# Kernel optimization log

Hardware: AMD Instinct MI355X
Metric: run time of the kernel (lower is better)

Reference implementation:

```python
import jax, jax.numpy as jnp
import numpy as np

B, IN, HID, H = 8192, 1024, 2048, 8
UP = 2 * IN          # input_size * proj_factor
HS = HID // H        # head size = 256
EPS = 1e-5


def _blockdiag(x, w, b):
    # x: [B, UP] -> chunk into H blocks of UP//H, per-block linear to HID//H
    xb = x.reshape(B, H, UP // H)
    y = jnp.einsum('bhi,hio->bho', xb, w)
    return y.reshape(B, HID) + b


def setup_inputs() -> dict:
    key = jax.random.key(0)
    ks = jax.random.split(key, 20)
    rn = lambda k, s: jax.random.normal(k, s, jnp.float32)
    p = lambda k, *s: rn(k, s) * 0.02
    return dict(
        x=rn(ks[0], (B, IN)),
        h_prev=rn(ks[1], (B, HID)), c_prev=rn(ks[2], (B, HID)),
        n_prev=rn(ks[3], (B, HID)), m_prev=rn(ks[4], (B, HID)),
        ln_g=jnp.ones(IN), ln_b=jnp.zeros(IN),
        w_ul=p(ks[5], IN, UP), b_ul=jnp.zeros(UP),
        w_ur=p(ks[6], IN, HID), b_ur=jnp.zeros(HID),
        conv_w=p(ks[7], 4), conv_b=jnp.zeros(()),
        w_skip=p(ks[8], UP, HID), b_skip=jnp.zeros(HID),
        w_q=p(ks[9], H, UP // H, HID // H), b_q=jnp.zeros(HID),
        w_k=p(ks[10], H, UP // H, HID // H), b_k=jnp.zeros(HID),
        w_v=p(ks[11], H, UP // H, HID // H), b_v=jnp.zeros(HID),
        w_i=p(ks[12], UP, HID), b_i=jnp.zeros(HID),
        w_f=p(ks[13], UP, HID), b_f=jnp.zeros(HID),
        w_o=p(ks[14], UP, HID), b_o=jnp.zeros(HID),
        gn_g=jnp.ones(HID), gn_b=jnp.zeros(HID),
        w_down=p(ks[15], HID, IN), b_down=jnp.zeros(IN),
    )


def reference(x, h_prev, c_prev, n_prev, m_prev, ln_g, ln_b,
              w_ul, b_ul, w_ur, b_ur, conv_w, conv_b, w_skip, b_skip,
              w_q, b_q, w_k, b_k, w_v, b_v, w_i, b_i, w_f, b_f, w_o, b_o,
              gn_g, gn_b, w_down, b_down):
    # LayerNorm over features
    mu = x.mean(-1, keepdims=True)
    var = x.var(-1, keepdims=True)
    xn = (x - mu) * jax.lax.rsqrt(var + EPS) * ln_g + ln_b

    xul = xn @ w_ul + b_ul          # [B, UP]
    xur = xn @ w_ur + b_ur          # [B, HID]

    # causal conv1d (kernel 4, 1 channel) along the feature axis, left-pad 3
    xp = jnp.pad(xul, ((0, 0), (3, 0)))
    xc = conv_b + sum(conv_w[j] * xp[:, j:j + UP] for j in range(4))
    xc = jax.nn.silu(xc)            # [B, UP]

    x_skip = xc @ w_skip + b_skip

    q = _blockdiag(xc, w_q, b_q)
    k = _blockdiag(xc, w_k, b_k) / np.sqrt(HS).astype(np.float32)
    v = _blockdiag(xul, w_v, b_v)

    i_t = xc @ w_i + b_i
    f_t = xc @ w_f + b_f
    o = jax.nn.sigmoid(xul @ w_o + b_o)

    m_t = jnp.maximum(f_t + m_prev, i_t)
    i = jnp.exp(i_t - m_t)
    f = jnp.exp(f_t + m_prev - m_t)
    c_t = f * c_prev + i * (v * k)
    n_t = f * n_prev + i * k

    denom = jnp.max(jnp.abs(n_t.T @ q), axis=1)     # [HID]
    h_t = o * (c_t * q) / denom

    # GroupNorm on (N, C), groups = H
    hg = h_t.reshape(B, H, HID // H)
    gm = hg.mean(-1, keepdims=True)
    gv = hg.var(-1, keepdims=True)
    hn = ((hg - gm) * jax.lax.rsqrt(gv + EPS)).reshape(B, HID) * gn_g + gn_b

    out = (hn + x_skip) * jax.nn.silu(xur)
    return out @ w_down + b_down + x, h_t, c_t, n_t, m_t
```

## Files before the change

### kernel.cpp

```cpp
#include <hip/hip_runtime.h>
#include <stdint.h>

#define B_    8192
#define IN_   1024
#define HID_  2048
#define UP_   2048
#define H_    8
#define HS_   256
#define EPS_  1e-5f

typedef __bf16 bf16x8 __attribute__((ext_vector_type(8)));
typedef float f32x4 __attribute__((ext_vector_type(4)));
typedef unsigned short u16x4 __attribute__((ext_vector_type(4)));
typedef unsigned short u16x8 __attribute__((ext_vector_type(8)));

__device__ __forceinline__ unsigned short f2bf(float f) {
  union { float f; unsigned int u; } v; v.f = f;
  unsigned int u = v.u;
  unsigned int r = (u + 0x7fffu + ((u >> 16) & 1u)) >> 16;
  return (unsigned short)r;
}
__device__ __forceinline__ float bf2f(unsigned short h) {
  union { unsigned int u; float f; } v; v.u = ((unsigned int)h) << 16;
  return v.f;
}

__device__ __forceinline__ void gload_lds16(const void* g, void* l) {
  auto gp = reinterpret_cast<const uint32_t __attribute__((address_space(1)))*>(
      reinterpret_cast<uintptr_t>(g));
  auto lp = reinterpret_cast<uint32_t __attribute__((address_space(3)))*>(
      reinterpret_cast<uintptr_t>(l));
  __builtin_amdgcn_global_load_lds(gp, lp, 16, 0, 0);
}

#define SB0 __builtin_amdgcn_sched_barrier(0)

#define PREFETCH_AF(DST, BASE, MI0)                                         \
  DST[0][0] = *(const bf16x8*)((BASE) + (aRdBase + (MI0) * 2048));          \
  DST[0][1] = *(const bf16x8*)((BASE) + ((aRdBase + (MI0) * 2048) ^ 64));   \
  DST[1][0] = *(const bf16x8*)((BASE) + (aRdBase + ((MI0) + 1) * 2048));    \
  DST[1][1] = *(const bf16x8*)((BASE) + ((aRdBase + ((MI0) + 1) * 2048) ^ 64));

#define LOAD_BFR(BASE)                                                      \
  _Pragma("unroll")                                                         \
  for (int ni = 0; ni < 4; ++ni) {                                          \
    bfr[ni][0] = *(const bf16x8*)((BASE) + (bRdBase + ni * 2048));          \
    bfr[ni][1] = *(const bf16x8*)((BASE) + ((bRdBase + ni * 2048) ^ 64));   \
  }

#define MFMA_CLUSTER(AF, Q)                                                 \
  __builtin_amdgcn_s_setprio(1);                                           \
  _Pragma("unroll")                                                         \
  for (int kq = 0; kq < 2; ++kq)                                            \
    _Pragma("unroll")                                                       \
    for (int m2 = 0; m2 < 2; ++m2)                                          \
      _Pragma("unroll")                                                     \
      for (int ni = 0; ni < 4; ++ni)                                        \
        acc[(Q) * 2 + m2][ni] = __builtin_amdgcn_mfma_f32_16x16x32_bf16(    \
            AF[m2][kq], bfr[ni][kq], acc[(Q) * 2 + m2][ni], 0, 0, 0);       \
  __builtin_amdgcn_s_setprio(0);

template <typename OutT, bool HAS_ADD>
__global__ __launch_bounds__(512, 2) void gemm8p(
    const unsigned short* __restrict__ A, int lda, int a_zoff,
    const unsigned short* __restrict__ W, int ldw, int w_zoff,
    const float* __restrict__ bias, const float* __restrict__ bias2,
    int bias_zoff,
    OutT* __restrict__ C, OutT* __restrict__ C2, int ldc, int c_zoff,
    int c_split,
    const float* __restrict__ ADD, float scale, float scale2, int K)
{
  __shared__ char lds[163840];
  const int z = blockIdx.z;
  A += (size_t)z * a_zoff;
  W += (size_t)z * w_zoff;
  if (bias) bias += (size_t)z * bias_zoff;
  if (bias2) bias2 += (size_t)z * bias_zoff;

  const int nwg = gridDim.x * gridDim.y;
  const int orig = blockIdx.y * gridDim.x + blockIdx.x;
  const int q8 = nwg >> 3, r8 = nwg & 7;
  const int xcd = orig & 7, xi = orig >> 3;
  const int wg = (xcd < r8 ? xcd * (q8 + 1) : r8 * (q8 + 1) + (xcd - r8) * q8) + xi;
  const int bx = wg % gridDim.x, by = wg / gridDim.x;

  const int t = threadIdx.x;
  const int lane = t & 63, wave = t >> 6;
  const int wr = wave >> 2, wc = wave & 3;
  const int l15 = lane & 15, l4 = lane >> 4;
  const int row0 = by * 256, col0 = bx * 256;

  const int lrow = lane >> 3;
  const int lslot = (lane & 7) ^ lrow;
  const size_t aLane = (size_t)lrow * lda * 2 + (size_t)lslot * 16;
  const size_t wLane = (size_t)lrow * ldw * 2 + (size_t)lslot * 16;
  const char* Abase = (const char*)A;
  const char* Wbase = (const char*)W;

  const int aRdBase = (wr * 128 + l15) * 128 + (((l4) ^ (l15 & 7)) * 16);
  const int bRdBase = (wc * 64 + l15) * 128 + (((l4) ^ (l15 & 7)) * 16);

  auto issueA = [&](int abuf, int half, int tile) {
#pragma unroll
    for (int j = 0; j < 2; ++j) {
      const int rbase = half * 128 + j * 64 + wave * 8;
      gload_lds16(Abase + (size_t)(row0 + rbase) * (lda * 2) + (size_t)tile * 128 + aLane,
                  lds + abuf * 32768 + rbase * 128 + lane * 16);
    }
  };
  auto issueB = [&](int bbuf, int half, int tile) {
#pragma unroll
    for (int j = 0; j < 2; ++j) {
      const int rbase = half * 128 + j * 64 + wave * 8;
      gload_lds16(Wbase + (size_t)(col0 + rbase) * (ldw * 2) + (size_t)tile * 128 + wLane,
                  lds + 98304 + bbuf * 32768 + rbase * 128 + lane * 16);
    }
  };

  f32x4 acc[8][4] = {};
  const int NT = K >> 6;

  bf16x8 bfr[4][2];
  bf16x8 afA[2][2], afB[2][2];

  issueA(0, 0, 0); issueA(0, 1, 0);
  issueB(0, 0, 0); issueB(0, 1, 0);
  if (NT > 1) {
    issueA(1, 0, 1); issueA(1, 1, 1);
    issueB(1, 0, 1); issueB(1, 1, 1);
    asm volatile("s_waitcnt vmcnt(8)" ::: "memory");
  } else {
    asm volatile("s_waitcnt vmcnt(0)" ::: "memory");
  }
  SB0;
  {
    const char* a0 = lds;
    const char* b0 = lds + 98304;
    LOAD_BFR(b0)
    PREFETCH_AF(afA, a0, 0)
    PREFETCH_AF(afB, a0, 2)
  }
  __builtin_amdgcn_s_barrier();
  SB0;

  for (int T = 0; T < NT; ++T) {
    const char* ldsA = lds + (T % 3) * 32768;
    const int abufN = (T + 2) % 3;
    const int bbufN = T & 1;
    asm volatile("s_waitcnt lgkmcnt(4)" ::: "memory"); SB0;
    MFMA_CLUSTER(afA, 0)
    PREFETCH_AF(afA, ldsA, 4)
    if (T + 2 < NT) issueA(abufN, 0, T + 2);
    asm volatile("s_waitcnt lgkmcnt(4)" ::: "memory"); SB0;
    MFMA_CLUSTER(afB, 1)
    __builtin_amdgcn_s_barrier();
    SB0;
    PREFETCH_AF(afB, ldsA, 6)
    if (T + 2 < NT) {
      issueA(abufN, 1, T + 2);
      issueB(bbufN, 0, T + 2);
      issueB(bbufN, 1, T + 2);
    }
    asm volatile("s_waitcnt lgkmcnt(4)" ::: "memory"); SB0;
    MFMA_CLUSTER(afA, 2)
    asm volatile("s_waitcnt lgkmcnt(0)" ::: "memory"); SB0;
    MFMA_CLUSTER(afB, 3)
    if (T + 2 < NT) asm volatile("s_waitcnt vmcnt(8)" ::: "memory");
    else            asm volatile("s_waitcnt vmcnt(0)" ::: "memory");
    SB0;
    if (T + 1 < NT) {
      const char* aN = lds + ((T + 1) % 3) * 32768;
      const char* bN = lds + 98304 + ((T + 1) & 1) * 32768;
      LOAD_BFR(bN)
      PREFETCH_AF(afA, aN, 0)
      PREFETCH_AF(afB, aN, 2)
    }
    __builtin_amdgcn_s_barrier();
    SB0;
  }

  const float* bp = bias;
  OutT* Cp = C;
  int cbase = col0;
  float sc = scale;
  if (col0 >= c_split) { bp = bias2; Cp = C2; cbase = col0 - c_split; sc = scale2; }
#pragma unroll
  for (int mi = 0; mi < 8; ++mi) {
#pragma unroll
    for (int ni = 0; ni < 4; ++ni) {
#pragma unroll
      for (int r = 0; r < 4; ++r) {
        const int m = row0 + wr * 128 + mi * 16 + l4 * 4 + r;
        const int n = wc * 64 + ni * 16 + l15;
        float v = acc[mi][ni][r];
        if (bp) v += bp[cbase + n];
        v *= sc;
        const size_t ci = (size_t)m * ldc + (size_t)z * c_zoff + cbase + n;
        if constexpr (HAS_ADD) v += ADD[ci];
        if constexpr (sizeof(OutT) == 2) Cp[ci] = (OutT)f2bf(v);
        else Cp[ci] = v;
      }
    }
  }
}

__global__ __launch_bounds__(256) void denom_reduce(
    const float* __restrict__ part, float* __restrict__ denom)
{
  const int m = blockIdx.x, t = threadIdx.x;
  const size_t P = (size_t)HID_ * HID_;
  float v = 0.f;
  for (int n = t; n < HID_; n += 256) {
    const size_t o = (size_t)m * HID_ + n;
    float s = part[o] + part[P + o] + part[2 * P + o] + part[3 * P + o];
    v = fmaxf(v, fabsf(s));
  }
#pragma unroll
  for (int off = 1; off < 64; off <<= 1) v = fmaxf(v, __shfl_xor(v, off, 64));
  __shared__ float red[4];
  if ((t & 63) == 0) red[t >> 6] = v;
  __syncthreads();
  if (t == 0) denom[m] = fmaxf(fmaxf(red[0], red[1]), fmaxf(red[2], red[3]));
}

__global__ __launch_bounds__(256) void down_reduce(
    const float* __restrict__ part, const float* __restrict__ x,
    const float* __restrict__ bias, float* __restrict__ out)
{
  const size_t idx = ((size_t)blockIdx.x * 256 + threadIdx.x) * 4;
  const size_t P = (size_t)B_ * IN_;
  f32x4 a = *(const f32x4*)(part + idx);
  f32x4 b = *(const f32x4*)(part + P + idx);
  f32x4 xv = *(const f32x4*)(x + idx);
  const int j = (int)(idx & (IN_ - 1));
  f32x4 bv = *(const f32x4*)(bias + j);
  f32x4 o;
#pragma unroll
  for (int e = 0; e < 4; ++e) o[e] = a[e] + b[e] + bv[e] + xv[e];
  *(f32x4*)(out + idx) = o;
}

template <typename InT>
__global__ __launch_bounds__(256) void transpose_bf(
    const InT* __restrict__ in, unsigned short* __restrict__ out, int R, int C,
    int izoff, int ozoff)
{
  __shared__ float tile[32][33];
  in += (size_t)blockIdx.z * izoff;
  out += (size_t)blockIdx.z * ozoff;
  const int cb = blockIdx.x * 32, rb = blockIdx.y * 32;
  const int tx = threadIdx.x, ty = threadIdx.y;
  for (int i = ty; i < 32; i += 8) {
    InT v = in[(size_t)(rb + i) * C + cb + tx];
    float f;
    if constexpr (sizeof(InT) == 2) f = bf2f((unsigned short)v);
    else f = (float)v;
    tile[i][tx] = f;
  }
  __syncthreads();
  for (int i = ty; i < 32; i += 8)
    out[(size_t)(cb + i) * R + rb + tx] = f2bf(tile[tx][i]);
}

__global__ __launch_bounds__(256) void ln_kernel(
    const float* __restrict__ x, const float* __restrict__ g,
    const float* __restrict__ b, unsigned short* __restrict__ xn)
{
  const int brow = blockIdx.x, t = threadIdx.x;
  const int lane = t & 63, wave = t >> 6;
  const float* xr = x + (size_t)brow * IN_;
  f32x4 v = *(const f32x4*)(xr + t * 4);
  float s = v[0] + v[1] + v[2] + v[3];
  float q = v[0]*v[0] + v[1]*v[1] + v[2]*v[2] + v[3]*v[3];
#pragma unroll
  for (int off = 32; off; off >>= 1) {
    s += __shfl_xor(s, off, 64);
    q += __shfl_xor(q, off, 64);
  }
  __shared__ float ss[4], sq[4];
  if (lane == 0) { ss[wave] = s; sq[wave] = q; }
  __syncthreads();
  s = ss[0] + ss[1] + ss[2] + ss[3];
  q = sq[0] + sq[1] + sq[2] + sq[3];
  const float mean = s * (1.f / IN_);
  const float var = q * (1.f / IN_) - mean * mean;
  const float rs = rsqrtf(var + EPS_);
  u16x4 o;
#pragma unroll
  for (int e = 0; e < 4; ++e) {
    const int j = t * 4 + e;
    o[e] = f2bf((v[e] - mean) * rs * g[j] + b[j]);
  }
  *(u16x4*)(xn + (size_t)brow * IN_ + t * 4) = o;
}

__global__ __launch_bounds__(256) void conv_kernel(
    const unsigned short* __restrict__ xul, const float* __restrict__ cw,
    const float* __restrict__ cb, unsigned short* __restrict__ xc)
{
  const int brow = blockIdx.x, t = threadIdx.x;
  const size_t base = (size_t)brow * UP_;
  const int j0 = t * 8;
  float xv[11];
#pragma unroll
  for (int e = 0; e < 11; ++e) {
    const int j = j0 + e - 3;
    xv[e] = (j >= 0) ? bf2f(xul[base + j]) : 0.f;
  }
  const float w0 = cw[0], w1 = cw[1], w2 = cw[2], w3 = cw[3], bb = cb[0];
  u16x8 o;
#pragma unroll
  for (int e = 0; e < 8; ++e) {
    float sv = bb + w0 * xv[e] + w1 * xv[e + 1] + w2 * xv[e + 2] + w3 * xv[e + 3];
    o[e] = f2bf(sv / (1.f + expf(-sv)));
  }
  *(u16x8*)(xc + base + j0) = o;
}

__global__ __launch_bounds__(256) void gates_kernel(
    const unsigned short* __restrict__ sif,
    const unsigned short* __restrict__ kb, const unsigned short* __restrict__ vb,
    const float* __restrict__ mprev, const float* __restrict__ cprev,
    const float* __restrict__ nprev,
    float* __restrict__ mo, float* __restrict__ co, float* __restrict__ no,
    unsigned short* __restrict__ nT)
{
  __shared__ unsigned short nt_t[64][72];
  const int t = threadIdx.x;
  const int r = t >> 2, cq = t & 3;
  const int row = blockIdx.y * 64 + r;
  const int colb = blockIdx.x * 64 + cq * 16;
  const size_t hidb = (size_t)row * HID_ + colb;
  const size_t sifb = (size_t)row * 6144 + colb;
#pragma unroll
  for (int e4 = 0; e4 < 4; ++e4) {
    const int c4 = e4 * 4;
    f32x4 mp = *(const f32x4*)(mprev + hidb + c4);
    f32x4 cp = *(const f32x4*)(cprev + hidb + c4);
    f32x4 np = *(const f32x4*)(nprev + hidb + c4);
    u16x4 iv = *(const u16x4*)(sif + sifb + 2048 + c4);
    u16x4 fv = *(const u16x4*)(sif + sifb + 4096 + c4);
    u16x4 kv = *(const u16x4*)(kb + hidb + c4);
    u16x4 vv = *(const u16x4*)(vb + hidb + c4);
    f32x4 mo4, co4, no4;
#pragma unroll
    for (int e = 0; e < 4; ++e) {
      const float ft = bf2f(fv[e]) + mp[e];
      const float it = bf2f(iv[e]);
      const float mt = fmaxf(ft, it);
      const float ie = expf(it - mt);
      const float fe = expf(ft - mt);
      const float k = bf2f(kv[e]), v = bf2f(vv[e]);
      mo4[e] = mt;
      co4[e] = fe * cp[e] + ie * (v * k);
      no4[e] = fe * np[e] + ie * k;
      nt_t[r][cq * 16 + c4 + e] = f2bf(no4[e]);
    }
    *(f32x4*)(mo + hidb + c4) = mo4;
    *(f32x4*)(co + hidb + c4) = co4;
    *(f32x4*)(no + hidb + c4) = no4;
  }
  __syncthreads();
  const int cT = t >> 2, sq = t & 3;
  u16x8 o0, o1;
#pragma unroll
  for (int e = 0; e < 8; ++e) {
    o0[e] = nt_t[sq * 16 + e][cT];
    o1[e] = nt_t[sq * 16 + 8 + e][cT];
  }
  const size_t ob = (size_t)(blockIdx.x * 64 + cT) * B_ + blockIdx.y * 64 + sq * 16;
  *(u16x8*)(nT + ob) = o0;
  *(u16x8*)(nT + ob + 8) = o1;
}

__global__ __launch_bounds__(256) void hgn_kernel(
    const float* __restrict__ ct, const unsigned short* __restrict__ olin,
    const unsigned short* __restrict__ qb, const float* __restrict__ denom,
    const unsigned short* __restrict__ sif, const unsigned short* __restrict__ xurb,
    const float* __restrict__ gng, const float* __restrict__ gnb,
    float* __restrict__ ho, unsigned short* __restrict__ pre)
{
  const int brow = blockIdx.x, t = threadIdx.x;
  const size_t base = (size_t)brow * HID_ + t * 8;
  u16x8 ov = *(const u16x8*)(olin + base);
  u16x8 qv = *(const u16x8*)(qb + base);
  f32x4 c0 = *(const f32x4*)(ct + base);
  f32x4 c1 = *(const f32x4*)(ct + base + 4);
  float h[8];
  float s = 0.f, sq = 0.f;
#pragma unroll
  for (int e = 0; e < 8; ++e) {
    const float o = 1.f / (1.f + expf(-bf2f(ov[e])));
    const float cv = (e < 4) ? c0[e] : c1[e - 4];
    const float hv = o * cv * bf2f(qv[e]) / denom[t * 8 + e];
    h[e] = hv; s += hv; sq += hv * hv;
  }
#pragma unroll
  for (int e = 0; e < 8; ++e) ho[base + e] = h[e];
#pragma unroll
  for (int off = 1; off < 32; off <<= 1) {
    s += __shfl_xor(s, off, 64);
    sq += __shfl_xor(sq, off, 64);
  }
  const float mean = s * (1.f / HS_);
  const float var = sq * (1.f / HS_) - mean * mean;
  const float rs = rsqrtf(var + EPS_);
  u16x8 sv = *(const u16x8*)(sif + (size_t)brow * 6144 + t * 8);
  u16x8 xv = *(const u16x8*)(xurb + base);
  u16x8 pv;
#pragma unroll
  for (int e = 0; e < 8; ++e) {
    const int j = t * 8 + e;
    const float hn = (h[e] - mean) * rs * gng[j] + gnb[j];
    const float xr = bf2f(xv[e]);
    const float sil = xr / (1.f + expf(-xr));
    pv[e] = f2bf((hn + bf2f(sv[e])) * sil);
  }
  *(u16x8*)(pre + base) = pv;
}

extern "C" void kernel_launch(void* const* d_in, const int* in_sizes, int n_in,
                              void* d_out, int out_size, void* d_ws, size_t ws_size,
                              hipStream_t stream)
{
  const float* x      = (const float*)d_in[0];
  const float* c_prev = (const float*)d_in[2];
  const float* n_prev = (const float*)d_in[3];
  const float* m_prev = (const float*)d_in[4];
  const float* ln_g   = (const float*)d_in[5];
  const float* ln_b   = (const float*)d_in[6];
  const float* w_ul   = (const float*)d_in[7];
  const float* b_ul   = (const float*)d_in[8];
  const float* w_ur   = (const float*)d_in[9];
  const float* b_ur   = (const float*)d_in[10];
  const float* conv_w = (const float*)d_in[11];
  const float* conv_b = (const float*)d_in[12];
  const float* w_skip = (const float*)d_in[13];
  const float* b_skip = (const float*)d_in[14];
  const float* w_q    = (const float*)d_in[15];
  const float* b_q    = (const float*)d_in[16];
  const float* w_k    = (const float*)d_in[17];
  const float* b_k    = (const float*)d_in[18];
  const float* w_v    = (const float*)d_in[19];
  const float* b_v    = (const float*)d_in[20];
  const float* w_i    = (const float*)d_in[21];
  const float* b_i    = (const float*)d_in[22];
  const float* w_f    = (const float*)d_in[23];
  const float* b_f    = (const float*)d_in[24];
  const float* w_o    = (const float*)d_in[25];
  const float* b_o    = (const float*)d_in[26];
  const float* gn_g   = (const float*)d_in[27];
  const float* gn_b   = (const float*)d_in[28];
  const float* w_down = (const float*)d_in[29];
  const float* b_down = (const float*)d_in[30];

  float* out_p = (float*)d_out;
  float* h_p = out_p + (size_t)B_ * IN_;
  float* c_p = h_p + (size_t)B_ * HID_;
  float* n_p = c_p + (size_t)B_ * HID_;
  float* m_p = n_p + (size_t)B_ * HID_;

  char* ws = (char*)d_ws;
  size_t off = 0;
  auto alloc = [&](size_t n) -> void* {
    void* p = ws + off;
    off += (n + 255) & ~(size_t)255;
    return p;
  };

  const size_t BH2 = (size_t)B_ * HID_ * 2;

  unsigned short* xn_bf   = (unsigned short*)alloc((size_t)B_ * IN_ * 2);
  unsigned short* xul_bf  = (unsigned short*)alloc(BH2);
  unsigned short* xur_bf  = (unsigned short*)alloc(BH2);
  unsigned short* xc_bf   = (unsigned short*)alloc(BH2);
  unsigned short* sif_bf  = (unsigned short*)alloc((size_t)B_ * 6144 * 2);
  unsigned short* q_bf    = (unsigned short*)alloc(BH2);
  unsigned short* k_bf    = (unsigned short*)alloc(BH2);
  unsigned short* v_bf    = (unsigned short*)alloc(BH2);
  unsigned short* olin_bf = (unsigned short*)alloc(BH2);
  unsigned short* qT_bf   = (unsigned short*)alloc(BH2);
  unsigned short* nT_bf   = (unsigned short*)alloc(BH2);
  unsigned short* pre_bf  = (unsigned short*)alloc(BH2);
  float* denom = (float*)alloc(HID_ * sizeof(float));
  float* part  = (float*)alloc((size_t)4 * HID_ * HID_ * sizeof(float));
  float* b_sif = (float*)alloc(6144 * sizeof(float));
  unsigned short* wt_ulur = (unsigned short*)alloc((size_t)4096 * IN_ * 2);
  unsigned short* wt_sif  = (unsigned short*)alloc((size_t)6144 * UP_ * 2);
  unsigned short* wt_qk   = (unsigned short*)alloc((size_t)H_ * 512 * HS_ * 2);
  unsigned short* wt_v    = (unsigned short*)alloc((size_t)H_ * HS_ * HS_ * 2);
  unsigned short* wt_o    = (unsigned short*)alloc((size_t)UP_ * HID_ * 2);
  unsigned short* wt_down = (unsigned short*)alloc((size_t)HID_ * IN_ * 2);

  if (off > ws_size) return;

  const dim3 tb32(32, 8);
  const int NOSPLIT = 1 << 30;

  hipMemcpyAsync(b_sif, b_skip, 2048 * 4, hipMemcpyDeviceToDevice, stream);
  hipMemcpyAsync(b_sif + 2048, b_i, 2048 * 4, hipMemcpyDeviceToDevice, stream);
  hipMemcpyAsync(b_sif + 4096, b_f, 2048 * 4, hipMemcpyDeviceToDevice, stream);

  transpose_bf<float><<<dim3(64, 32, 1), tb32, 0, stream>>>(w_ul, wt_ulur, 1024, 2048, 0, 0);
  transpose_bf<float><<<dim3(64, 32, 1), tb32, 0, stream>>>(w_ur, wt_ulur + (size_t)2048 * 1024, 1024, 2048, 0, 0);
  transpose_bf<float><<<dim3(64, 64, 1), tb32, 0, stream>>>(w_skip, wt_sif, 2048, 2048, 0, 0);
  transpose_bf<float><<<dim3(64, 64, 1), tb32, 0, stream>>>(w_i, wt_sif + (size_t)2048 * 2048, 2048, 2048, 0, 0);
  transpose_bf<float><<<dim3(64, 64, 1), tb32, 0, stream>>>(w_f, wt_sif + (size_t)4096 * 2048, 2048, 2048, 0, 0);
  transpose_bf<float><<<dim3(8, 8, 8), tb32, 0, stream>>>(w_q, wt_qk, 256, 256, 65536, 131072);
  transpose_bf<float><<<dim3(8, 8, 8), tb32, 0, stream>>>(w_k, wt_qk + 65536, 256, 256, 65536, 131072);
  transpose_bf<float><<<dim3(8, 8, 8), tb32, 0, stream>>>(w_v, wt_v, 256, 256, 65536, 65536);
  transpose_bf<float><<<dim3(64, 64, 1), tb32, 0, stream>>>(w_o, wt_o, 2048, 2048, 0, 0);
  transpose_bf<float><<<dim3(32, 64, 1), tb32, 0, stream>>>(w_down, wt_down, 2048, 1024, 0, 0);

  ln_kernel<<<B_, 256, 0, stream>>>(x, ln_g, ln_b, xn_bf);

  gemm8p<unsigned short, false><<<dim3(16, 32, 1), 512, 0, stream>>>(
      xn_bf, IN_, 0, wt_ulur, IN_, 0, b_ul, b_ur, 0,
      xul_bf, xur_bf, HID_, 0, 2048, nullptr, 1.f, 1.f, IN_);

  conv_kernel<<<B_, 256, 0, stream>>>(xul_bf, conv_w, conv_b, xc_bf);

  gemm8p<unsigned short, false><<<dim3(24, 32, 1), 512, 0, stream>>>(
      xc_bf, UP_, 0, wt_sif, UP_, 0, b_sif, nullptr, 0,
      sif_bf, sif_bf, 6144, 0, NOSPLIT, nullptr, 1.f, 1.f, UP_);

  gemm8p<unsigned short, false><<<dim3(2, 32, 8), 512, 0, stream>>>(
      xc_bf, UP_, HS_, wt_qk, HS_, 512 * HS_, b_q, b_k, HS_,
      q_bf, k_bf, HID_, HS_, 256, nullptr, 1.f, 0.0625f, HS_);

  gemm8p<unsigned short, false><<<dim3(1, 32, 8), 512, 0, stream>>>(
      xul_bf, UP_, HS_, wt_v, HS_, HS_ * HS_, b_v, nullptr, HS_,
      v_bf, v_bf, HID_, HS_, NOSPLIT, nullptr, 1.f, 1.f, HS_);

  gemm8p<unsigned short, false><<<dim3(8, 32, 1), 512, 0, stream>>>(
      xul_bf, UP_, 0, wt_o, UP_, 0, b_o, nullptr, 0,
      olin_bf, olin_bf, HID_, 0, NOSPLIT, nullptr, 1.f, 1.f, UP_);

  gates_kernel<<<dim3(HID_ / 64, B_ / 64, 1), 256, 0, stream>>>(
      sif_bf, k_bf, v_bf, m_prev, c_prev, n_prev, m_p, c_p, n_p, nT_bf);

  transpose_bf<unsigned short><<<dim3(64, 256, 1), tb32, 0, stream>>>(
      q_bf, qT_bf, B_, HID_, 0, 0);

  gemm8p<float, false><<<dim3(8, 8, 4), 512, 0, stream>>>(
      nT_bf, B_, B_ / 4, qT_bf, B_, B_ / 4, nullptr, nullptr, 0,
      part, part, HID_, HID_ * HID_, NOSPLIT, nullptr, 1.f, 1.f, B_ / 4);
  denom_reduce<<<HID_, 256, 0, stream>>>(part, denom);

  hgn_kernel<<<B_, 256, 0, stream>>>(
      c_p, olin_bf, q_bf, denom, sif_bf, xur_bf, gn_g, gn_b, h_p, pre_bf);

  gemm8p<float, false><<<dim3(4, 32, 2), 512, 0, stream>>>(
      pre_bf, UP_, 1024, wt_down, UP_, 1024, nullptr, nullptr, 0,
      part, part, IN_, B_ * IN_, NOSPLIT, nullptr, 1.f, 1.f, 1024);
  down_reduce<<<(B_ * IN_ / 4) / 256, 256, 0, stream>>>(part, x, b_down, out_p);
}
```

Before: 992.8 us.

## Batch weight transposes, fuse q transpose into gates kernel, group GEMM tile order

Replaces ten separate weight-transpose launches with one kernel that picks the source matrix from the block index. Folds the q transpose into the gates kernel through a second LDS tile, removing a separate pass that re-read q. Remaps GEMM workgroups into groups of 8 row tiles so neighbouring blocks share A rows and get better L2 reuse. Adds more LDS per gates block and branchy index math in the transpose kernel.

New measurement: 975.4 us. Within noise of the previous version (-1.7%).

```diff
diff --git a/kernel.cpp b/kernel.cpp
--- a/kernel.cpp
+++ b/kernel.cpp
@@ -77,12 +77,23 @@
   if (bias) bias += (size_t)z * bias_zoff;
   if (bias2) bias2 += (size_t)z * bias_zoff;
 
-  const int nwg = gridDim.x * gridDim.y;
-  const int orig = blockIdx.y * gridDim.x + blockIdx.x;
+  const int gx = gridDim.x, gy = gridDim.y;
+  const int nwg = gx * gy;
+  const int orig = blockIdx.y * gx + blockIdx.x;
   const int q8 = nwg >> 3, r8 = nwg & 7;
   const int xcd = orig & 7, xi = orig >> 3;
   const int wg = (xcd < r8 ? xcd * (q8 + 1) : r8 * (q8 + 1) + (xcd - r8) * q8) + xi;
-  const int bx = wg % gridDim.x, by = wg / gridDim.x;
+  int bx, by;
+  if ((gy & 7) == 0) {
+    const int per = gx * 8;
+    const int g0 = (wg / per) * 8;
+    const int rem = wg % per;
+    bx = rem >> 3;
+    by = g0 + (rem & 7);
+  } else {
+    bx = wg % gx;
+    by = wg / gx;
+  }
 
   const int t = threadIdx.x;
   const int lane = t & 63, wave = t >> 6;
@@ -240,23 +251,38 @@
   *(f32x4*)(out + idx) = o;
 }
 
-template <typename InT>
-__global__ __launch_bounds__(256) void transpose_bf(
-    const InT* __restrict__ in, unsigned short* __restrict__ out, int R, int C,
-    int izoff, int ozoff)
+struct TP {
+  const float* src[10];
+  unsigned short* dst[10];
+};
+
+__global__ __launch_bounds__(256) void transpose_all(TP p)
 {
   __shared__ float tile[32][33];
-  in += (size_t)blockIdx.z * izoff;
-  out += (size_t)blockIdx.z * ozoff;
-  const int cb = blockIdx.x * 32, rb = blockIdx.y * 32;
-  const int tx = threadIdx.x, ty = threadIdx.y;
-  for (int i = ty; i < 32; i += 8) {
-    InT v = in[(size_t)(rb + i) * C + cb + tx];
-    float f;
-    if constexpr (sizeof(InT) == 2) f = bf2f((unsigned short)v);
-    else f = (float)v;
-    tile[i][tx] = f;
-  }
+  const int tid = blockIdx.x;
+  int w, base, R, C, izoff, ozoff;
+  if      (tid < 2048)  { w = 0; base = 0;     R = 1024; C = 2048; izoff = 0;     ozoff = 0; }
+  else if (tid < 4096)  { w = 1; base = 2048;  R = 1024; C = 2048; izoff = 0;     ozoff = 0; }
+  else if (tid < 8192)  { w = 2; base = 4096;  R = 2048; C = 2048; izoff = 0;     ozoff = 0; }
+  else if (tid < 12288) { w = 3; base = 8192;  R = 2048; C = 2048; izoff = 0;     ozoff = 0; }
+  else if (tid < 16384) { w = 4; base = 12288; R = 2048; C = 2048; izoff = 0;     ozoff = 0; }
+  else if (tid < 16896) { w = 5; base = 16384; R = 256;  C = 256;  izoff = 65536; ozoff = 131072; }
+  else if (tid < 17408) { w = 6; base = 16896; R = 256;  C = 256;  izoff = 65536; ozoff = 131072; }
+  else if (tid < 17920) { w = 7; base = 17408; R = 256;  C = 256;  izoff = 65536; ozoff = 65536; }
+  else if (tid < 22016) { w = 8; base = 17920; R = 2048; C = 2048; izoff = 0;     ozoff = 0; }
+  else                  { w = 9; base = 22016; R = 2048; C = 1024; izoff = 0;     ozoff = 0; }
+  const int local = tid - base;
+  const int cx = C >> 5;
+  const int tpz = cx * (R >> 5);
+  const int z = local / tpz;
+  const int rem = local % tpz;
+  const int bx = rem % cx, by = rem / cx;
+  const float* in = p.src[w] + (size_t)z * izoff;
+  unsigned short* out = p.dst[w] + (size_t)z * ozoff;
+  const int cb = bx * 32, rb = by * 32;
+  const int tx = threadIdx.x & 31, ty = threadIdx.x >> 5;
+  for (int i = ty; i < 32; i += 8)
+    tile[i][tx] = in[(size_t)(rb + i) * C + cb + tx];
   __syncthreads();
   for (int i = ty; i < 32; i += 8)
     out[(size_t)(cb + i) * R + rb + tx] = f2bf(tile[tx][i]);
@@ -320,12 +346,14 @@
 __global__ __launch_bounds__(256) void gates_kernel(
     const unsigned short* __restrict__ sif,
     const unsigned short* __restrict__ kb, const unsigned short* __restrict__ vb,
+    const unsigned short* __restrict__ qb,
     const float* __restrict__ mprev, const float* __restrict__ cprev,
     const float* __restrict__ nprev,
     float* __restrict__ mo, float* __restrict__ co, float* __restrict__ no,
-    unsigned short* __restrict__ nT)
+    unsigned short* __restrict__ nT, unsigned short* __restrict__ qT)
 {
   __shared__ unsigned short nt_t[64][72];
+  __shared__ unsigned short qt_t[64][72];
   const int t = threadIdx.x;
   const int r = t >> 2, cq = t & 3;
   const int row = blockIdx.y * 64 + r;
@@ -342,6 +370,7 @@
     u16x4 fv = *(const u16x4*)(sif + sifb + 4096 + c4);
     u16x4 kv = *(const u16x4*)(kb + hidb + c4);
     u16x4 vv = *(const u16x4*)(vb + hidb + c4);
+    u16x4 qv = *(const u16x4*)(qb + hidb + c4);
     f32x4 mo4, co4, no4;
 #pragma unroll
     for (int e = 0; e < 4; ++e) {
@@ -355,6 +384,7 @@
       co4[e] = fe * cp[e] + ie * (v * k);
       no4[e] = fe * np[e] + ie * k;
       nt_t[r][cq * 16 + c4 + e] = f2bf(no4[e]);
+      qt_t[r][cq * 16 + c4 + e] = qv[e];
     }
     *(f32x4*)(mo + hidb + c4) = mo4;
     *(f32x4*)(co + hidb + c4) = co4;
@@ -362,15 +392,19 @@
   }
   __syncthreads();
   const int cT = t >> 2, sq = t & 3;
-  u16x8 o0, o1;
+  u16x8 o0, o1, p0, p1;
 #pragma unroll
   for (int e = 0; e < 8; ++e) {
     o0[e] = nt_t[sq * 16 + e][cT];
     o1[e] = nt_t[sq * 16 + 8 + e][cT];
+    p0[e] = qt_t[sq * 16 + e][cT];
+    p1[e] = qt_t[sq * 16 + 8 + e][cT];
   }
   const size_t ob = (size_t)(blockIdx.x * 64 + cT) * B_ + blockIdx.y * 64 + sq * 16;
   *(u16x8*)(nT + ob) = o0;
   *(u16x8*)(nT + ob + 8) = o1;
+  *(u16x8*)(qT + ob) = p0;
+  *(u16x8*)(qT + ob + 8) = p1;
 }
 
 __global__ __launch_bounds__(256) void hgn_kernel(
@@ -494,23 +528,24 @@
 
   if (off > ws_size) return;
 
-  const dim3 tb32(32, 8);
   const int NOSPLIT = 1 << 30;
 
   hipMemcpyAsync(b_sif, b_skip, 2048 * 4, hipMemcpyDeviceToDevice, stream);
   hipMemcpyAsync(b_sif + 2048, b_i, 2048 * 4, hipMemcpyDeviceToDevice, stream);
   hipMemcpyAsync(b_sif + 4096, b_f, 2048 * 4, hipMemcpyDeviceToDevice, stream);
 
-  transpose_bf<float><<<dim3(64, 32, 1), tb32, 0, stream>>>(w_ul, wt_ulur, 1024, 2048, 0, 0);
-  transpose_bf<float><<<dim3(64, 32, 1), tb32, 0, stream>>>(w_ur, wt_ulur + (size_t)2048 * 1024, 1024, 2048, 0, 0);
-  transpose_bf<float><<<dim3(64, 64, 1), tb32, 0, stream>>>(w_skip, wt_sif, 2048, 2048, 0, 0);
-  transpose_bf<float><<<dim3(64, 64, 1), tb32, 0, stream>>>(w_i, wt_sif + (size_t)2048 * 2048, 2048, 2048, 0, 0);
-  transpose_bf<float><<<dim3(64, 64, 1), tb32, 0, stream>>>(w_f, wt_sif + (size_t)4096 * 2048, 2048, 2048, 0, 0);
-  transpose_bf<float><<<dim3(8, 8, 8), tb32, 0, stream>>>(w_q, wt_qk, 256, 256, 65536, 131072);
-  transpose_bf<float><<<dim3(8, 8, 8), tb32, 0, stream>>>(w_k, wt_qk + 65536, 256, 256, 65536, 131072);
-  transpose_bf<float><<<dim3(8, 8, 8), tb32, 0, stream>>>(w_v, wt_v, 256, 256, 65536, 65536);
-  transpose_bf<float><<<dim3(64, 64, 1), tb32, 0, stream>>>(w_o, wt_o, 2048, 2048, 0, 0);
-  transpose_bf<float><<<dim3(32, 64, 1), tb32, 0, stream>>>(w_down, wt_down, 2048, 1024, 0, 0);
+  TP tp;
+  tp.src[0] = w_ul;   tp.dst[0] = wt_ulur;
+  tp.src[1] = w_ur;   tp.dst[1] = wt_ulur + (size_t)2048 * 1024;
+  tp.src[2] = w_skip; tp.dst[2] = wt_sif;
+  tp.src[3] = w_i;    tp.dst[3] = wt_sif + (size_t)2048 * 2048;
+  tp.src[4] = w_f;    tp.dst[4] = wt_sif + (size_t)4096 * 2048;
+  tp.src[5] = w_q;    tp.dst[5] = wt_qk;
+  tp.src[6] = w_k;    tp.dst[6] = wt_qk + 65536;
+  tp.src[7] = w_v;    tp.dst[7] = wt_v;
+  tp.src[8] = w_o;    tp.dst[8] = wt_o;
+  tp.src[9] = w_down; tp.dst[9] = wt_down;
+  transpose_all<<<24064, 256, 0, stream>>>(tp);
 
   ln_kernel<<<B_, 256, 0, stream>>>(x, ln_g, ln_b, xn_bf);
 
@@ -537,10 +572,8 @@
       olin_bf, olin_bf, HID_, 0, NOSPLIT, nullptr, 1.f, 1.f, UP_);
 
   gates_kernel<<<dim3(HID_ / 64, B_ / 64, 1), 256, 0, stream>>>(
-      sif_bf, k_bf, v_bf, m_prev, c_prev, n_prev, m_p, c_p, n_p, nT_bf);
-
-  transpose_bf<unsigned short><<<dim3(64, 256, 1), tb32, 0, stream>>>(
-      q_bf, qT_bf, B_, HID_, 0, 0);
+      sif_bf, k_bf, v_bf, q_bf, m_prev, c_prev, n_prev,
+      m_p, c_p, n_p, nT_bf, qT_bf);
 
   gemm8p<float, false><<<dim3(8, 8, 4), 512, 0, stream>>>(
       nT_bf, B_, B_ / 4, qT_bf, B_, B_ / 4, nullptr, nullptr, 0,
```
